# Kernel tuning notes

Measured on AMD Instinct MI355X. Metric: run time of the kernel, lower is better.

## Reference

```python
import jax, jax.numpy as jnp
import numpy as np

N_HEAD = 16
WINDOW = 256


def setup_inputs() -> dict:
    key = jax.random.key(0)
    ks = jax.random.split(key, 3)
    B, S, D = 2, 2048, 1024
    x = jax.random.normal(ks[0], (B, S, D), dtype=jnp.float32)
    w_attn = jax.random.normal(ks[1], (D, 3 * D), dtype=jnp.float32) * 0.02
    b_attn = jnp.zeros((3 * D,), dtype=jnp.float32)
    w_proj = jax.random.normal(ks[2], (D, D), dtype=jnp.float32) * 0.02
    b_proj = jnp.zeros((D,), dtype=jnp.float32)
    return {"x": x, "w_attn": w_attn, "b_attn": b_attn, "w_proj": w_proj, "b_proj": b_proj}


def reference(x, w_attn, b_attn, w_proj, b_proj):
    B, S, D = x.shape
    hd = D // N_HEAD  # head dim
    scale = 1.0 / np.sqrt(hd).astype(np.float32)

    # fused QKV projection (Conv1D == linear on last dim)
    c = jnp.einsum('bsd,df->bsf', x, w_attn) + b_attn
    q, k, v = jnp.split(c, 3, axis=-1)

    def split_heads(t):  # [B,S,D] -> [B,H,S,hd]
        return t.reshape(B, S, N_HEAD, hd).transpose(0, 2, 1, 3)

    q, k, v = split_heads(q), split_heads(k), split_heads(v)
    present = jnp.stack([k, v], axis=1)  # [B,2,H,S,hd]

    # scores [B,H,S,S]
    w = jnp.einsum('bhqd,bhkd->bhqk', q, k) * scale

    # causal sliding-window mask
    q_pos = jnp.arange(S)[:, None]
    k_pos = jnp.arange(S)[None, :]
    mask = (k_pos <= q_pos) & (k_pos >= q_pos - WINDOW + 1)  # [S,S]
    w = jnp.where(mask[None, None], w, jnp.finfo(w.dtype).min)
    w = jax.nn.softmax(w, axis=-1)

    a = jnp.einsum('bhqk,bhkd->bhqd', w, v)
    a = a.transpose(0, 2, 1, 3).reshape(B, S, D)  # merge heads
    out = jnp.einsum('bsd,df->bsf', a, w_proj) + b_proj
    return out, present
```

## Files before the change

### kernel.cpp

```cpp
#include <hip/hip_runtime.h>
#include <cstdint>
#include <cstddef>

typedef __bf16 bf16x8 __attribute__((ext_vector_type(8)));
typedef float f32x4 __attribute__((ext_vector_type(4)));

#define MFMA16(a, b, c) __builtin_amdgcn_mfma_f32_16x16x32_bf16(a, b, c, 0, 0, 0)

static __device__ __forceinline__ bf16x8 ld_bf16x8(const __bf16* p) {
    return *reinterpret_cast<const bf16x8*>(p);
}

static __device__ __forceinline__ void async_cp16(const __bf16* g, __bf16* l) {
    __builtin_amdgcn_global_load_lds((const __attribute__((address_space(1))) void*)g,
                                     (__attribute__((address_space(3))) void*)l, 16, 0, 0);
}

template <int N>
static __device__ __forceinline__ void wait_vmcnt() {
    asm volatile("s_waitcnt vmcnt(%0)" ::"n"(N) : "memory");
}

__global__ void cvt_kernel(const float* __restrict__ src, __bf16* __restrict__ dst, int n8) {
    int i = blockIdx.x * blockDim.x + threadIdx.x;
    if (i >= n8) return;
    const float4* s4 = reinterpret_cast<const float4*>(src) + (size_t)i * 2;
    float4 a = s4[0], b = s4[1];
    bf16x8 o;
    o[0] = (__bf16)a.x; o[1] = (__bf16)a.y; o[2] = (__bf16)a.z; o[3] = (__bf16)a.w;
    o[4] = (__bf16)b.x; o[5] = (__bf16)b.y; o[6] = (__bf16)b.z; o[7] = (__bf16)b.w;
    reinterpret_cast<bf16x8*>(dst)[i] = o;
}

__global__ __launch_bounds__(256) void tcvt_kernel(const float* __restrict__ in,
                                                   __bf16* __restrict__ out, int K, int N) {
    __shared__ __bf16 T[64][72];
    const int k0 = blockIdx.y * 64, n0 = blockIdx.x * 64;
    const int t = threadIdx.x;
    const int col = (t & 15) << 2;
    const int rowb = t >> 4;
    #pragma unroll
    for (int i = 0; i < 4; i++) {
        int row = i * 16 + rowb;
        float4 v = *reinterpret_cast<const float4*>(&in[(size_t)(k0 + row) * N + n0 + col]);
        T[col + 0][row] = (__bf16)v.x;
        T[col + 1][row] = (__bf16)v.y;
        T[col + 2][row] = (__bf16)v.z;
        T[col + 3][row] = (__bf16)v.w;
    }
    __syncthreads();
    const int oc = (t & 7) << 3;
    const int orb = t >> 3;
    #pragma unroll
    for (int i = 0; i < 2; i++) {
        int r = i * 32 + orb;
        bf16x8 v = *reinterpret_cast<bf16x8*>(&T[r][oc]);
        *reinterpret_cast<bf16x8*>(&out[(size_t)(n0 + r) * K + k0 + oc]) = v;
    }
}

template <int BM, int BN, int WM, int WN>
__device__ __forceinline__ void mainloop2(const __bf16* __restrict__ A,
                                          const __bf16* __restrict__ Bt,
                                          int K, int row0, int col0,
                                          __bf16* lds,
                                          f32x4 (&acc)[BM / WM / 16][BN / WN / 16]) {
    constexpr int MR = BM / WM / 16, NR = BN / WN / 16;
    constexpr int AE = BM * 32;
    constexpr int BUFE = AE + BN * 32;
    constexpr int AI = BM / 16;
    constexpr int BI = BN / 16;
    constexpr int APW = AI / 8;
    constexpr int BPW = BI / 8;
    constexpr int BSPLIT = BI - BPW * 8;
    const int tid = threadIdx.x, l = tid & 63, w = tid >> 6;
    const int wm = w / WN, wn = w % WN;
    const int lr = l >> 2, lc = (l & 3) << 3;
    const int fr = l & 15, fc = (l >> 4) << 3;

    const size_t arow = (size_t)(row0 + lr) * K + lc;
    const size_t brow = (size_t)(col0 + lr) * K + lc;
    const int nt = K >> 5;

    auto stage = [&](int t, int buf) {
        const int k0 = t << 5;
        const int bb = buf * BUFE;
        #pragma unroll
        for (int j = 0; j < APW; j++) {
            const int mi = w * APW + j;
            async_cp16(A + arow + (size_t)mi * 16 * K + k0, lds + bb + mi * 512 + l * 8);
        }
        if (BSPLIT == 0) {
            #pragma unroll
            for (int j = 0; j < BPW; j++) {
                const int ni = w * BPW + j;
                async_cp16(Bt + brow + (size_t)ni * 16 * K + k0, lds + bb + AE + ni * 512 + l * 8);
            }
        } else if (w < BSPLIT) {
            #pragma unroll
            for (int j = 0; j < BPW + 1; j++) {
                const int ni = w * (BPW + 1) + j;
                async_cp16(Bt + brow + (size_t)ni * 16 * K + k0, lds + bb + AE + ni * 512 + l * 8);
            }
        } else {
            #pragma unroll
            for (int j = 0; j < BPW; j++) {
                const int ni = BSPLIT * (BPW + 1) + (w - BSPLIT) * BPW + j;
                async_cp16(Bt + brow + (size_t)ni * 16 * K + k0, lds + bb + AE + ni * 512 + l * 8);
            }
        }
    };

    stage(0, 0);
    stage(1, 1);

    const int aoff = (wm * (BM / WM) + fr) * 32 + fc;
    const int boff = AE + (wn * (BN / WN) + fr) * 32 + fc;

    int p = 0;
    for (int t = 0; t < nt; ++t) {
        if (t + 1 < nt) {
            if (BSPLIT != 0 && w < BSPLIT) wait_vmcnt<APW + BPW + 1>();
            else wait_vmcnt<APW + BPW>();
        } else {
            wait_vmcnt<0>();
        }
        __builtin_amdgcn_sched_barrier(0);
        __builtin_amdgcn_s_barrier();
        __builtin_amdgcn_sched_barrier(0);
        if (t + 2 < nt) {
            int p2 = p + 2; if (p2 >= 3) p2 -= 3;
            stage(t + 2, p2);
        }
        const int cb = p * BUFE;
        bf16x8 af[MR], bfv[NR];
        #pragma unroll
        for (int m = 0; m < MR; m++) af[m] = ld_bf16x8(&lds[cb + aoff + m * 512]);
        #pragma unroll
        for (int n = 0; n < NR; n++) bfv[n] = ld_bf16x8(&lds[cb + boff + n * 512]);
        __builtin_amdgcn_s_setprio(1);
        #pragma unroll
        for (int m = 0; m < MR; m++) {
            #pragma unroll
            for (int n = 0; n < NR; n++) {
                acc[m][n] = MFMA16(af[m], bfv[n], acc[m][n]);
            }
        }
        __builtin_amdgcn_s_setprio(0);
        asm volatile("s_waitcnt lgkmcnt(0)" ::: "memory");
        __builtin_amdgcn_sched_barrier(0);
        p = (p == 2) ? 0 : p + 1;
    }
}

__global__ __launch_bounds__(512, 2) void gemm_qkv_kernel(const __bf16* __restrict__ xb,
                                                          const __bf16* __restrict__ wabt,
                                                          const float* __restrict__ bias,
                                                          __bf16* __restrict__ qb,
                                                          __bf16* __restrict__ kb,
                                                          __bf16* __restrict__ vt,
                                                          float* __restrict__ present) {
    __shared__ __bf16 lds[3 * (256 * 32 + 192 * 32)];
    f32x4 acc[8][3] = {};
    const int row0 = blockIdx.y * 256, col0 = blockIdx.x * 192;
    mainloop2<256, 192, 2, 4>(xb, wabt, 1024, row0, col0, lds, acc);

    const int lane = threadIdx.x & 63, w = threadIdx.x >> 6;
    const int wm = w >> 2, wn = w & 3;
    #pragma unroll
    for (int n = 0; n < 3; n++) {
        int col = col0 + wn * 48 + n * 16 + (lane & 15);
        int part = col >> 10;
        int hh = (col >> 6) & 15;
        int dd = col & 63;
        float bv = bias[col];
        #pragma unroll
        for (int m = 0; m < 8; m++) {
            #pragma unroll
            for (int r = 0; r < 4; r++) {
                int row = row0 + wm * 128 + m * 16 + ((lane >> 4) << 2) + r;
                int bb = row >> 11, ss = row & 2047;
                float val = acc[m][n][r] + bv;
                size_t qi = (((size_t)(bb * 16 + hh)) * 2048 + ss) * 64 + dd;
                if (part == 0) {
                    qb[qi] = (__bf16)val;
                } else if (part == 1) {
                    kb[qi] = (__bf16)val;
                    present[(((size_t)((bb * 2 + 0) * 16 + hh)) * 2048 + ss) * 64 + dd] = val;
                } else {
                    vt[(((size_t)(bb * 16 + hh)) * 64 + dd) * 2048 + ss] = (__bf16)val;
                    present[(((size_t)((bb * 2 + 1) * 16 + hh)) * 2048 + ss) * 64 + dd] = val;
                }
            }
        }
    }
}

__global__ __launch_bounds__(512, 2) void gemm_proj_kernel(const __bf16* __restrict__ ab,
                                                           const __bf16* __restrict__ wpbt,
                                                           const float* __restrict__ bias,
                                                           float* __restrict__ out) {
    __shared__ __bf16 lds[3 * (128 * 32 + 128 * 32)];
    f32x4 acc[2][4] = {};
    const int row0 = blockIdx.y * 128, col0 = blockIdx.x * 128;
    mainloop2<128, 128, 4, 2>(ab, wpbt, 1024, row0, col0, lds, acc);

    const int lane = threadIdx.x & 63, w = threadIdx.x >> 6;
    const int wm = w >> 1, wn = w & 1;
    #pragma unroll
    for (int n = 0; n < 4; n++) {
        int col = col0 + wn * 64 + n * 16 + (lane & 15);
        float bv = bias[col];
        #pragma unroll
        for (int m = 0; m < 2; m++) {
            #pragma unroll
            for (int r = 0; r < 4; r++) {
                int row = row0 + wm * 32 + m * 16 + ((lane >> 4) << 2) + r;
                out[(size_t)row * 1024 + col] = acc[m][n][r] + bv;
            }
        }
    }
}

__global__ __launch_bounds__(256) void attn_kernel(const __bf16* __restrict__ qb,
                                                   const __bf16* __restrict__ kb,
                                                   const __bf16* __restrict__ vtb,
                                                   __bf16* __restrict__ ab) {
    __shared__ __bf16 Pls[4][16 * 40];
    const int bh = blockIdx.x >> 5;
    const int qt = blockIdx.x & 31;
    const int lane = threadIdx.x & 63, wid = threadIdx.x >> 6;
    const int q0w = qt * 64 + wid * 16;

    const __bf16* Qh = qb + (size_t)bh * 2048 * 64;
    const __bf16* Kh = kb + (size_t)bh * 2048 * 64;
    const __bf16* Vt = vtb + (size_t)bh * 64 * 2048;
    __bf16* Pw = &Pls[wid][0];

    bf16x8 qf[2];
    {
        int qr = q0w + (lane & 15);
        const __bf16* qp = Qh + (size_t)qr * 64 + ((lane >> 4) << 3);
        qf[0] = ld_bf16x8(qp);
        qf[1] = ld_bf16x8(qp + 32);
    }

    f32x4 o[4];
    #pragma unroll
    for (int dt = 0; dt < 4; dt++) o[dt] = (f32x4){0.f, 0.f, 0.f, 0.f};
    float mrun[4] = {-1e30f, -1e30f, -1e30f, -1e30f};
    float srun[4] = {0.f, 0.f, 0.f, 0.f};

    const float scale = 0.125f;
    int klo = q0w - 255;
    int kt0 = klo > 0 ? (klo & ~31) : 0;

    for (int kt = kt0; kt <= q0w + 15; kt += 32) {
        f32x4 s[2];
        #pragma unroll
        for (int kc = 0; kc < 2; kc++) {
            int krow = kt + kc * 16 + (lane & 15);
            const __bf16* kp = Kh + (size_t)krow * 64 + ((lane >> 4) << 3);
            bf16x8 kf0 = ld_bf16x8(kp);
            bf16x8 kf1 = ld_bf16x8(kp + 32);
            f32x4 a = (f32x4){0.f, 0.f, 0.f, 0.f};
            a = MFMA16(qf[0], kf0, a);
            a = MFMA16(qf[1], kf1, a);
            s[kc] = a;
        }
        float p0v[4], p1v[4], factor[4];
        #pragma unroll
        for (int r = 0; r < 4; r++) {
            int q = q0w + ((lane >> 4) << 2) + r;
            int k0i = kt + (lane & 15);
            int k1i = k0i + 16;
            bool ok0 = (k0i <= q) && (k0i > q - 256);
            bool ok1 = (k1i <= q) && (k1i > q - 256);
            float s0 = ok0 ? s[0][r] * scale : -1e30f;
            float s1 = ok1 ? s[1][r] * scale : -1e30f;
            float mx = fmaxf(s0, s1);
            #pragma unroll
            for (int off = 1; off < 16; off <<= 1) mx = fmaxf(mx, __shfl_xor(mx, off));
            float mn = fmaxf(mrun[r], mx);
            float f = __expf(mrun[r] - mn);
            float p0 = ok0 ? __expf(s0 - mn) : 0.f;
            float p1 = ok1 ? __expf(s1 - mn) : 0.f;
            float ps = p0 + p1;
            #pragma unroll
            for (int off = 1; off < 16; off <<= 1) ps += __shfl_xor(ps, off);
            srun[r] = srun[r] * f + ps;
            mrun[r] = mn;
            factor[r] = f;
            p0v[r] = p0;
            p1v[r] = p1;
        }
        #pragma unroll
        for (int dt = 0; dt < 4; dt++) {
            #pragma unroll
            for (int r = 0; r < 4; r++) o[dt][r] *= factor[r];
        }
        #pragma unroll
        for (int r = 0; r < 4; r++) {
            int qrow = ((lane >> 4) << 2) + r;
            Pw[qrow * 40 + (lane & 15)] = (__bf16)p0v[r];
            Pw[qrow * 40 + 16 + (lane & 15)] = (__bf16)p1v[r];
        }
        asm volatile("s_waitcnt lgkmcnt(0)" ::: "memory");
        bf16x8 pf = ld_bf16x8(&Pw[(lane & 15) * 40 + ((lane >> 4) << 3)]);
        #pragma unroll
        for (int dt = 0; dt < 4; dt++) {
            bf16x8 vf = ld_bf16x8(&Vt[(size_t)(dt * 16 + (lane & 15)) * 2048 + kt + ((lane >> 4) << 3)]);
            o[dt] = MFMA16(pf, vf, o[dt]);
        }
    }

    const int bb = bh >> 4, hh = bh & 15;
    #pragma unroll
    for (int r = 0; r < 4; r++) {
        int q = q0w + ((lane >> 4) << 2) + r;
        float inv = 1.f / srun[r];
        size_t base = ((size_t)bb * 2048 + q) * 1024 + hh * 64;
        #pragma unroll
        for (int dt = 0; dt < 4; dt++) {
            ab[base + dt * 16 + (lane & 15)] = (__bf16)(o[dt][r] * inv);
        }
    }
}

extern "C" void kernel_launch(void* const* d_in, const int* in_sizes, int n_in,
                              void* d_out, int out_size, void* d_ws, size_t ws_size,
                              hipStream_t stream) {
    const float* x = (const float*)d_in[0];
    const float* w_attn = (const float*)d_in[1];
    const float* b_attn = (const float*)d_in[2];
    const float* w_proj = (const float*)d_in[3];
    const float* b_proj = (const float*)d_in[4];

    float* out = (float*)d_out;
    float* present = out + (size_t)2 * 2048 * 1024;

    char* w = (char*)d_ws;
    __bf16* xb   = (__bf16*)(w);
    __bf16* wabt = (__bf16*)(w + 8388608);
    __bf16* wpbt = (__bf16*)(w + 14680064);
    __bf16* qb   = (__bf16*)(w + 16777216);
    __bf16* kb   = (__bf16*)(w + 25165824);
    __bf16* vt   = (__bf16*)(w + 33554432);
    __bf16* ab   = xb;

    cvt_kernel<<<2048, 256, 0, stream>>>(x, xb, 524288);
    tcvt_kernel<<<dim3(48, 16), 256, 0, stream>>>(w_attn, wabt, 1024, 3072);
    tcvt_kernel<<<dim3(16, 16), 256, 0, stream>>>(w_proj, wpbt, 1024, 1024);

    gemm_qkv_kernel<<<dim3(16, 16), 512, 0, stream>>>(xb, wabt, b_attn, qb, kb, vt, present);

    attn_kernel<<<1024, 256, 0, stream>>>(qb, kb, vt, ab);

    gemm_proj_kernel<<<dim3(8, 32), 512, 0, stream>>>(ab, wpbt, b_proj, out);
}
```

Baseline: 124.0 us.

## Use smaller 128x128 QKV GEMM tiles and streamline attention softmax with DPP reductions

The QKV projection GEMM moves from a 256x192 tile, 512-thread, triple-buffered mainloop to a simpler 128x128 tile, 256-thread, double-buffered mainloop. That launches 768 blocks instead of 256, trading per-block reuse for better CU fill. The attention softmax now uses DPP row reductions instead of shuffle-xor, exp2 with a pre-folded log2e scale, and a mask-free fast path for fully in-window key tiles. The new GEMM syncs more often and reuses each loaded tile less.

```diff
diff --git a/kernel.cpp b/kernel.cpp
--- a/kernel.cpp
+++ b/kernel.cpp
@@ -19,6 +19,32 @@
 template <int N>
 static __device__ __forceinline__ void wait_vmcnt() {
     asm volatile("s_waitcnt vmcnt(%0)" ::"n"(N) : "memory");
+}
+
+static __device__ __forceinline__ void barrier_pinned() {
+    __builtin_amdgcn_sched_barrier(0);
+    __builtin_amdgcn_s_barrier();
+    __builtin_amdgcn_sched_barrier(0);
+}
+
+template <int CTRL>
+static __device__ __forceinline__ float dppmv(float x) {
+    return __builtin_bit_cast(float, __builtin_amdgcn_update_dpp(
+        0, __builtin_bit_cast(int, x), CTRL, 0xF, 0xF, true));
+}
+static __device__ __forceinline__ float rmax16(float x) {
+    x = fmaxf(x, dppmv<0x121>(x));
+    x = fmaxf(x, dppmv<0x122>(x));
+    x = fmaxf(x, dppmv<0x124>(x));
+    x = fmaxf(x, dppmv<0x128>(x));
+    return x;
+}
+static __device__ __forceinline__ float rsum16(float x) {
+    x += dppmv<0x121>(x);
+    x += dppmv<0x122>(x);
+    x += dppmv<0x124>(x);
+    x += dppmv<0x128>(x);
+    return x;
 }
 
 __global__ void cvt_kernel(const float* __restrict__ src, __bf16* __restrict__ dst, int n8) {
@@ -56,6 +82,102 @@
         int r = i * 32 + orb;
         bf16x8 v = *reinterpret_cast<bf16x8*>(&T[r][oc]);
         *reinterpret_cast<bf16x8*>(&out[(size_t)(n0 + r) * K + k0 + oc]) = v;
+    }
+}
+
+__device__ __forceinline__ void gemm_mainloop(const __bf16* __restrict__ A,
+                                              const __bf16* __restrict__ Bt,
+                                              int K, int row0, int col0,
+                                              __bf16* Als, __bf16* Bls, f32x4 acc[4][4]) {
+    const int tid = threadIdx.x;
+    const int lane = tid & 63;
+    const int wid = tid >> 6;
+    const int wr = wid >> 1, wc = wid & 1;
+    const int r0 = tid >> 2, o0 = (tid & 3) << 3;
+    const __bf16* a0 = A + (size_t)(row0 + r0) * K + o0;
+    const __bf16* a1 = A + (size_t)(row0 + r0 + 64) * K + o0;
+    const __bf16* b0 = Bt + (size_t)(col0 + r0) * K + o0;
+    const __bf16* b1 = Bt + (size_t)(col0 + r0 + 64) * K + o0;
+    const int loff = tid * 8;
+    const int aoff = (wr * 64 + (lane & 15)) * 32 + ((lane >> 4) << 3);
+    const int boff = (wc * 64 + (lane & 15)) * 32 + ((lane >> 4) << 3);
+
+    const int nt = K >> 5;
+    async_cp16(a0, &Als[loff]);
+    async_cp16(a1, &Als[loff + 2048]);
+    async_cp16(b0, &Bls[loff]);
+    async_cp16(b1, &Bls[loff + 2048]);
+    __syncthreads();
+
+    int cur = 0;
+    for (int t = 0; t < nt; ++t) {
+        if (t + 1 < nt) {
+            const int k1 = (t + 1) << 5;
+            const int nb = (cur ^ 1) * 4096;
+            async_cp16(a0 + k1, &Als[nb + loff]);
+            async_cp16(a1 + k1, &Als[nb + loff + 2048]);
+            async_cp16(b0 + k1, &Bls[nb + loff]);
+            async_cp16(b1 + k1, &Bls[nb + loff + 2048]);
+        }
+        const int cb = cur * 4096;
+        bf16x8 af[4], bfr[4];
+        #pragma unroll
+        for (int m = 0; m < 4; m++) af[m] = ld_bf16x8(&Als[cb + aoff + m * 512]);
+        #pragma unroll
+        for (int n = 0; n < 4; n++) bfr[n] = ld_bf16x8(&Bls[cb + boff + n * 512]);
+        #pragma unroll
+        for (int m = 0; m < 4; m++) {
+            #pragma unroll
+            for (int n = 0; n < 4; n++) {
+                acc[m][n] = MFMA16(af[m], bfr[n], acc[m][n]);
+            }
+        }
+        __syncthreads();
+        cur ^= 1;
+    }
+}
+
+__global__ __launch_bounds__(256) void gemm_qkv_kernel(const __bf16* __restrict__ xb,
+                                                       const __bf16* __restrict__ wabt,
+                                                       const float* __restrict__ bias,
+                                                       __bf16* __restrict__ qb,
+                                                       __bf16* __restrict__ kb,
+                                                       __bf16* __restrict__ vt,
+                                                       float* __restrict__ present) {
+    __shared__ __bf16 Als[2 * 128 * 32];
+    __shared__ __bf16 Bls[2 * 128 * 32];
+    f32x4 acc[4][4] = {};
+    const int row0 = blockIdx.y * 128, col0 = blockIdx.x * 128;
+    gemm_mainloop(xb, wabt, 1024, row0, col0, Als, Bls, acc);
+
+    const int lane = threadIdx.x & 63, wid = threadIdx.x >> 6;
+    const int wr = wid >> 1, wc = wid & 1;
+    const int part = col0 >> 10;
+    #pragma unroll
+    for (int n = 0; n < 4; n++) {
+        int col = col0 + wc * 64 + n * 16 + (lane & 15);
+        int hh = (col >> 6) & 15;
+        int dd = col & 63;
+        float bv = bias[col];
+        #pragma unroll
+        for (int m = 0; m < 4; m++) {
+            #pragma unroll
+            for (int r = 0; r < 4; r++) {
+                int row = row0 + wr * 64 + m * 16 + ((lane >> 4) << 2) + r;
+                int bb = row >> 11, ss = row & 2047;
+                float val = acc[m][n][r] + bv;
+                size_t qi = (((size_t)(bb * 16 + hh)) * 2048 + ss) * 64 + dd;
+                if (part == 0) {
+                    qb[qi] = (__bf16)val;
+                } else if (part == 1) {
+                    kb[qi] = (__bf16)val;
+                    present[(((size_t)((bb * 2 + 0) * 16 + hh)) * 2048 + ss) * 64 + dd] = val;
+                } else {
+                    vt[(((size_t)(bb * 16 + hh)) * 64 + dd) * 2048 + ss] = (__bf16)val;
+                    present[(((size_t)((bb * 2 + 1) * 16 + hh)) * 2048 + ss) * 64 + dd] = val;
+                }
+            }
+        }
     }
 }
 
@@ -72,7 +194,6 @@
     constexpr int BI = BN / 16;
     constexpr int APW = AI / 8;
     constexpr int BPW = BI / 8;
-    constexpr int BSPLIT = BI - BPW * 8;
     const int tid = threadIdx.x, l = tid & 63, w = tid >> 6;
     const int wm = w / WN, wn = w % WN;
     const int lr = l >> 2, lc = (l & 3) << 3;
@@ -90,24 +211,10 @@
             const int mi = w * APW + j;
             async_cp16(A + arow + (size_t)mi * 16 * K + k0, lds + bb + mi * 512 + l * 8);
         }
-        if (BSPLIT == 0) {
-            #pragma unroll
-            for (int j = 0; j < BPW; j++) {
-                const int ni = w * BPW + j;
-                async_cp16(Bt + brow + (size_t)ni * 16 * K + k0, lds + bb + AE + ni * 512 + l * 8);
-            }
-        } else if (w < BSPLIT) {
-            #pragma unroll
-            for (int j = 0; j < BPW + 1; j++) {
-                const int ni = w * (BPW + 1) + j;
-                async_cp16(Bt + brow + (size_t)ni * 16 * K + k0, lds + bb + AE + ni * 512 + l * 8);
-            }
-        } else {
-            #pragma unroll
-            for (int j = 0; j < BPW; j++) {
-                const int ni = BSPLIT * (BPW + 1) + (w - BSPLIT) * BPW + j;
-                async_cp16(Bt + brow + (size_t)ni * 16 * K + k0, lds + bb + AE + ni * 512 + l * 8);
-            }
+        #pragma unroll
+        for (int j = 0; j < BPW; j++) {
+            const int ni = w * BPW + j;
+            async_cp16(Bt + brow + (size_t)ni * 16 * K + k0, lds + bb + AE + ni * 512 + l * 8);
         }
     };
 
@@ -120,14 +227,11 @@
     int p = 0;
     for (int t = 0; t < nt; ++t) {
         if (t + 1 < nt) {
-            if (BSPLIT != 0 && w < BSPLIT) wait_vmcnt<APW + BPW + 1>();
-            else wait_vmcnt<APW + BPW>();
+            wait_vmcnt<APW + BPW>();
         } else {
             wait_vmcnt<0>();
         }
-        __builtin_amdgcn_sched_barrier(0);
-        __builtin_amdgcn_s_barrier();
-        __builtin_amdgcn_sched_barrier(0);
+        barrier_pinned();
         if (t + 2 < nt) {
             int p2 = p + 2; if (p2 >= 3) p2 -= 3;
             stage(t + 2, p2);
@@ -150,49 +254,6 @@
         asm volatile("s_waitcnt lgkmcnt(0)" ::: "memory");
         __builtin_amdgcn_sched_barrier(0);
         p = (p == 2) ? 0 : p + 1;
-    }
-}
-
-__global__ __launch_bounds__(512, 2) void gemm_qkv_kernel(const __bf16* __restrict__ xb,
-                                                          const __bf16* __restrict__ wabt,
-                                                          const float* __restrict__ bias,
-                                                          __bf16* __restrict__ qb,
-                                                          __bf16* __restrict__ kb,
-                                                          __bf16* __restrict__ vt,
-                                                          float* __restrict__ present) {
-    __shared__ __bf16 lds[3 * (256 * 32 + 192 * 32)];
-    f32x4 acc[8][3] = {};
-    const int row0 = blockIdx.y * 256, col0 = blockIdx.x * 192;
-    mainloop2<256, 192, 2, 4>(xb, wabt, 1024, row0, col0, lds, acc);
-
-    const int lane = threadIdx.x & 63, w = threadIdx.x >> 6;
-    const int wm = w >> 2, wn = w & 3;
-    #pragma unroll
-    for (int n = 0; n < 3; n++) {
-        int col = col0 + wn * 48 + n * 16 + (lane & 15);
-        int part = col >> 10;
-        int hh = (col >> 6) & 15;
-        int dd = col & 63;
-        float bv = bias[col];
-        #pragma unroll
-        for (int m = 0; m < 8; m++) {
-            #pragma unroll
-            for (int r = 0; r < 4; r++) {
-                int row = row0 + wm * 128 + m * 16 + ((lane >> 4) << 2) + r;
-                int bb = row >> 11, ss = row & 2047;
-                float val = acc[m][n][r] + bv;
-                size_t qi = (((size_t)(bb * 16 + hh)) * 2048 + ss) * 64 + dd;
-                if (part == 0) {
-                    qb[qi] = (__bf16)val;
-                } else if (part == 1) {
-                    kb[qi] = (__bf16)val;
-                    present[(((size_t)((bb * 2 + 0) * 16 + hh)) * 2048 + ss) * 64 + dd] = val;
-                } else {
-                    vt[(((size_t)(bb * 16 + hh)) * 64 + dd) * 2048 + ss] = (__bf16)val;
-                    present[(((size_t)((bb * 2 + 1) * 16 + hh)) * 2048 + ss) * 64 + dd] = val;
-                }
-            }
-        }
     }
 }
 
@@ -251,7 +312,7 @@
     float mrun[4] = {-1e30f, -1e30f, -1e30f, -1e30f};
     float srun[4] = {0.f, 0.f, 0.f, 0.f};
 
-    const float scale = 0.125f;
+    const float cl2 = 0.18033688f;
     int klo = q0w - 255;
     int kt0 = klo > 0 ? (klo & ~31) : 0;
 
@@ -268,31 +329,47 @@
             a = MFMA16(qf[1], kf1, a);
             s[kc] = a;
         }
+        const bool clean = (kt >= q0w - 240) && (kt + 31 <= q0w);
         float p0v[4], p1v[4], factor[4];
-        #pragma unroll
-        for (int r = 0; r < 4; r++) {
-            int q = q0w + ((lane >> 4) << 2) + r;
-            int k0i = kt + (lane & 15);
-            int k1i = k0i + 16;
-            bool ok0 = (k0i <= q) && (k0i > q - 256);
-            bool ok1 = (k1i <= q) && (k1i > q - 256);
-            float s0 = ok0 ? s[0][r] * scale : -1e30f;
-            float s1 = ok1 ? s[1][r] * scale : -1e30f;
-            float mx = fmaxf(s0, s1);
-            #pragma unroll
-            for (int off = 1; off < 16; off <<= 1) mx = fmaxf(mx, __shfl_xor(mx, off));
-            float mn = fmaxf(mrun[r], mx);
-            float f = __expf(mrun[r] - mn);
-            float p0 = ok0 ? __expf(s0 - mn) : 0.f;
-            float p1 = ok1 ? __expf(s1 - mn) : 0.f;
-            float ps = p0 + p1;
-            #pragma unroll
-            for (int off = 1; off < 16; off <<= 1) ps += __shfl_xor(ps, off);
-            srun[r] = srun[r] * f + ps;
-            mrun[r] = mn;
-            factor[r] = f;
-            p0v[r] = p0;
-            p1v[r] = p1;
+        if (clean) {
+            #pragma unroll
+            for (int r = 0; r < 4; r++) {
+                float s0 = s[0][r] * cl2;
+                float s1 = s[1][r] * cl2;
+                float mx = rmax16(fmaxf(s0, s1));
+                float mn = fmaxf(mrun[r], mx);
+                float f = exp2f(mrun[r] - mn);
+                float p0 = exp2f(s0 - mn);
+                float p1 = exp2f(s1 - mn);
+                float ps = rsum16(p0 + p1);
+                srun[r] = srun[r] * f + ps;
+                mrun[r] = mn;
+                factor[r] = f;
+                p0v[r] = p0;
+                p1v[r] = p1;
+            }
+        } else {
+            #pragma unroll
+            for (int r = 0; r < 4; r++) {
+                int q = q0w + ((lane >> 4) << 2) + r;
+                int k0i = kt + (lane & 15);
+                int k1i = k0i + 16;
+                bool ok0 = (k0i <= q) && (k0i > q - 256);
+                bool ok1 = (k1i <= q) && (k1i > q - 256);
+                float s0 = ok0 ? s[0][r] * cl2 : -1e30f;
+                float s1 = ok1 ? s[1][r] * cl2 : -1e30f;
+                float mx = rmax16(fmaxf(s0, s1));
+                float mn = fmaxf(mrun[r], mx);
+                float f = exp2f(mrun[r] - mn);
+                float p0 = ok0 ? exp2f(s0 - mn) : 0.f;
+                float p1 = ok1 ? exp2f(s1 - mn) : 0.f;
+                float ps = rsum16(p0 + p1);
+                srun[r] = srun[r] * f + ps;
+                mrun[r] = mn;
+                factor[r] = f;
+                p0v[r] = p0;
+                p1v[r] = p1;
+            }
         }
         #pragma unroll
         for (int dt = 0; dt < 4; dt++) {
@@ -352,7 +429,7 @@
     tcvt_kernel<<<dim3(48, 16), 256, 0, stream>>>(w_attn, wabt, 1024, 3072);
     tcvt_kernel<<<dim3(16, 16), 256, 0, stream>>>(w_proj, wpbt, 1024, 1024);
 
-    gemm_qkv_kernel<<<dim3(16, 16), 512, 0, stream>>>(xb, wabt, b_attn, qb, kb, vt, present);
+    gemm_qkv_kernel<<<dim3(24, 32), 256, 0, stream>>>(xb, wabt, b_attn, qb, kb, vt, present);
 
     attn_kernel<<<1024, 256, 0, stream>>>(qb, kb, vt, ab);
 
```

After: 121.7 us. No clear change (-1.8%).
